# Kernel tuning notes

Measured on AMD Instinct MI355X. Metric: run time of the kernel, lower is better.

The kernel has to match this reference:

```python
import jax, jax.numpy as jnp
import numpy as np

DIM = 3
N = DIM * DIM          # 9 digits
NUM_NODES = N * N      # 81 cells
HID = 96
EMB = 16

def sudoku_edges():
    edges = []
    for r in range(N):
        for c in range(N):
            s = set()
            for k in range(N):
                s.add(r * N + k)
                s.add(k * N + c)
            br, bc = (r // DIM) * DIM, (c // DIM) * DIM
            for dr in range(DIM):
                for dc in range(DIM):
                    s.add((br + dr) * N + (bc + dc))
            s.discard(r * N + c)
            edges.append(sorted(s))
    return np.asarray(edges, np.int32)  # (81, 20)

EDGES = jnp.asarray(sudoku_edges())

def mlp(x, params):
    # ReLU between hidden layers, no activation after the last layer
    for w, b in params[:-1]:
        x = jax.nn.relu(x @ w + b)
    w, b = params[-1]
    return x @ w + b

def setup_inputs():
    key = jax.random.key(0)
    ks = iter(jax.random.split(key, 64))
    B = 256
    def p(shape, scale=0.1):
        return jax.random.normal(next(ks), shape, jnp.float32) * scale
    inp = {}
    inp['grids'] = jax.random.randint(next(ks), (B, NUM_NODES), 0, 3)
    inp['iters'] = 8
    inp['emb'] = p((3, EMB))
    inp['in_w0'] = p((EMB, HID)); inp['in_b0'] = jnp.zeros((HID,), jnp.float32)
    inp['in_w1'] = p((HID, HID)); inp['in_b1'] = jnp.zeros((HID,), jnp.float32)
    inp['in_w2'] = p((HID, HID)); inp['in_b2'] = jnp.zeros((HID,), jnp.float32)
    inp['rel_w0'] = p((2 * HID, HID)); inp['rel_b0'] = jnp.zeros((HID,), jnp.float32)
    inp['rel_w1'] = p((HID, HID)); inp['rel_b1'] = jnp.zeros((HID,), jnp.float32)
    inp['rel_w2'] = p((HID, HID)); inp['rel_b2'] = jnp.zeros((HID,), jnp.float32)
    inp['g_w0'] = p((2 * HID, HID)); inp['g_b0'] = jnp.zeros((HID,), jnp.float32)
    inp['g_w1'] = p((HID, HID)); inp['g_b1'] = jnp.zeros((HID,), jnp.float32)
    inp['g_w2'] = p((HID, HID)); inp['g_b2'] = jnp.zeros((HID,), jnp.float32)
    inp['lstm_wih'] = p((HID, 4 * HID)); inp['lstm_whh'] = p((HID, 4 * HID))
    inp['lstm_bih'] = jnp.zeros((4 * HID,), jnp.float32)
    inp['lstm_bhh'] = jnp.zeros((4 * HID,), jnp.float32)
    inp['r_w0'] = p((HID, HID)); inp['r_b0'] = jnp.zeros((HID,), jnp.float32)
    inp['r_w1'] = p((HID, HID)); inp['r_b1'] = jnp.zeros((HID,), jnp.float32)
    inp['r_w2'] = p((HID, N)); inp['r_b2'] = jnp.zeros((N,), jnp.float32)
    inp['c0'] = p((B * NUM_NODES, HID), 1.0)  # torch.randn LSTM cell init
    return inp

def reference(grids, iters, emb, in_w0, in_b0, in_w1, in_b1, in_w2, in_b2,
              rel_w0, rel_b0, rel_w1, rel_b1, rel_w2, rel_b2,
              g_w0, g_b0, g_w1, g_b1, g_w2, g_b2,
              lstm_wih, lstm_whh, lstm_bih, lstm_bhh,
              r_w0, r_b0, r_w1, r_b1, r_w2, r_b2, c0):
    B = grids.shape[0]
    in_p = [(in_w0, in_b0), (in_w1, in_b1), (in_w2, in_b2)]
    rel_p = [(rel_w0, rel_b0), (rel_w1, rel_b1), (rel_w2, rel_b2)]
    g_p = [(g_w0, g_b0), (g_w1, g_b1), (g_w2, g_b2)]
    r_p = [(r_w0, r_b0), (r_w1, r_b1), (r_w2, r_b2)]
    X = mlp(emb[grids], in_p)                     # (B, 81, 96)
    H0 = jax.lax.stop_gradient(X)                 # X.clone().detach()
    h = H0.reshape(B * NUM_NODES, HID)
    bias = lstm_bih + lstm_bhh

    def step(carry, _):
        h, c = carry
        Hn = h.reshape(B, NUM_NODES, HID)
        nbr = Hn[:, EDGES]                        # (B, 81, 20, 96) neighbor gather
        self_f = jnp.broadcast_to(Hn[:, :, None], nbr.shape)
        msgs = mlp(jnp.concatenate([self_f, nbr], axis=-1), rel_p)
        M = msgs.sum(axis=2)                      # scatter-sum of messages
        x_in = mlp(jnp.concatenate([X, M], axis=-1), g_p).reshape(B * NUM_NODES, HID)
        gates = x_in @ lstm_wih + h @ lstm_whh + bias
        i, f, g, o = jnp.split(gates, 4, axis=-1)  # torch gate order i,f,g,o
        c2 = jax.nn.sigmoid(f) * c + jax.nn.sigmoid(i) * jnp.tanh(g)
        h2 = jax.nn.sigmoid(o) * jnp.tanh(c2)
        out = mlp(h2.reshape(B, NUM_NODES, HID), r_p)  # (B, 81, 9)
        return (h2, c2), out

    _, outputs = jax.lax.scan(step, (h, c0), None, length=iters)
    return outputs  # (iters, B, 81, 9)
```

## Files before the change

kernel.cpp:

```cpp
#include <hip/hip_runtime.h>
#include <hip/hip_bf16.h>
#include <stdint.h>

typedef __attribute__((ext_vector_type(8))) short short8v;
typedef __attribute__((ext_vector_type(4))) float float4v;

#define DEVI __device__ __forceinline__

constexpr int BATCH = 256;
constexpr int NN   = 81;
constexpr int HID  = 96;
constexpr int NOUT = 9;
constexpr int BLOCK = 512;
constexpr int LDA = 100;
constexpr int LDB = 104;

constexpr int OFF_XG = 0;
constexpr int OFF_H0 = 7776;
constexpr int OFF_H1 = 11988;
constexpr int OFF_MS = 16200;
constexpr int OFF_AP = 24300;
constexpr int OFF_BV = 32400;
constexpr int SMEM_F = 40500;

constexpr int W_REL0A = 0;
constexpr int W_REL0B = 18432;
constexpr int W_REL1  = 36864;
constexpr int W_COMB  = 55296;
constexpr int W_G1    = 73728;
constexpr int W_IHC   = 92160;
constexpr int W_HH    = 165888;
constexpr int W_R0    = 239616;
constexpr int W_R1    = 258048;
constexpr int W_R2    = 276480;
constexpr int W_IN1   = 279552;
constexpr int W_IN2   = 297984;
constexpr int W_G0A   = 316416;
constexpr int BC2OFF  = 334848;
constexpr int B3OFF   = 335616;

DEVI float sigm(float x)  { return 1.f / (1.f + __expf(-x)); }
DEVI float tanh_(float x) { return 1.f - 2.f / (__expf(2.f * x) + 1.f); }

DEVI short bfhi(float x) { union { float f; unsigned u; } v; v.f = x; return (short)(v.u >> 16); }
DEVI float fromBits(short s) { union { unsigned u; float f; } v; v.u = ((unsigned)(unsigned short)s) << 16; return v.f; }
DEVI short bfrne(float x) {
  union { float f; unsigned u; } v; v.f = x;
  unsigned r = v.u + 0x7fffu + ((v.u >> 16) & 1u);
  return (short)(r >> 16);
}
DEVI void split1(float x, short& h, short& l) { h = bfhi(x); l = bfrne(x - fromBits(h)); }

DEVI void packFrag(const float* p, short8v& v) {
  const float4 a = *reinterpret_cast<const float4*>(p);
  const float4 b = *reinterpret_cast<const float4*>(p + 4);
  v[0] = bfrne(a.x); v[1] = bfrne(a.y); v[2] = bfrne(a.z); v[3] = bfrne(a.w);
  v[4] = bfrne(b.x); v[5] = bfrne(b.y); v[6] = bfrne(b.z); v[7] = bfrne(b.w);
}
DEVI void packFragPair(const float* ap, const float* bp, short8v& v) {
  const float4 a0 = *reinterpret_cast<const float4*>(ap);
  const float4 a1 = *reinterpret_cast<const float4*>(ap + 4);
  const float4 b0 = *reinterpret_cast<const float4*>(bp);
  const float4 b1 = *reinterpret_cast<const float4*>(bp + 4);
  v[0] = bfrne(fmaxf(a0.x + b0.x, 0.f)); v[1] = bfrne(fmaxf(a0.y + b0.y, 0.f));
  v[2] = bfrne(fmaxf(a0.z + b0.z, 0.f)); v[3] = bfrne(fmaxf(a0.w + b0.w, 0.f));
  v[4] = bfrne(fmaxf(a1.x + b1.x, 0.f)); v[5] = bfrne(fmaxf(a1.y + b1.y, 0.f));
  v[6] = bfrne(fmaxf(a1.z + b1.z, 0.f)); v[7] = bfrne(fmaxf(a1.w + b1.w, 0.f));
}

DEVI float4v mfma2(short8v a, short8v bh, short8v bl, float4v acc) {
  acc = __builtin_amdgcn_mfma_f32_16x16x32_bf16(a, bh, acc, 0, 0, 0);
  acc = __builtin_amdgcn_mfma_f32_16x16x32_bf16(a, bl, acc, 0, 0, 0);
  return acc;
}

DEVI int nbr_of(int n, int e) {
  const int r = n / 9, c = n - 9 * r;
  if (e < 8)  { int cc = c + 1 + e;  if (cc >= 9) cc -= 9; return r * 9 + cc; }
  if (e < 16) { int rr = r + e - 7;  if (rr >= 9) rr -= 9; return rr * 9 + c; }
  const int q = e - 16, dr = 1 + (q >> 1), dc = 1 + (q & 1);
  const int rm = r % 3, cm = c % 3;
  int rr = r - rm + rm + dr; rr -= (rm + dr >= 3) ? 3 : 0;
  int cc = c - cm + cm + dc; cc -= (cm + dc >= 3) ? 3 : 0;
  return rr * 9 + cc;
}

__global__ __launch_bounds__(64)
void pack_kernel(const float* rel_w0, const float* rel_w1, const float* rel_w2,
                 const float* g_w0, const float* g_w1, const float* g_w2,
                 const float* wih, const float* whh,
                 const float* r_w0, const float* r_w1, const float* r_w2,
                 const float* in_w1, const float* in_w2,
                 const float* rel_b2, const float* g_b2, short* ws)
{
  const int lane = threadIdx.x;
  const int blk = blockIdx.x;
  if (blk == 327) {
    float* bc2 = reinterpret_cast<float*>(ws + BC2OFF);
    float* b3  = reinterpret_cast<float*>(ws + B3OFF);
    for (int c = lane; c < 384; c += 64) {
      float a = 0.f;
      for (int t = 0; t < 96; ++t) a += g_b2[t] * wih[t * 384 + c];
      bc2[c] = a;
    }
    for (int c = lane; c < 96; c += 64) {
      float a = 0.f;
      for (int t = 0; t < 96; ++t) a += 20.f * rel_b2[t] * g_w0[(96 + t) * 96 + c];
      b3[c] = a;
    }
    return;
  }
  const int starts[14] = {0,18,36,54,72,90,162,234,252,270,273,291,309,327};
  int mi = 0;
  while (blk >= starts[mi + 1]) ++mi;
  const int tt = blk - starts[mi];
  const int ntile = starts[mi + 1] - starts[mi];
  const int kt = tt % 3, ct = tt / 3;
  const int q = lane >> 4, r = lane & 15;
  int off, C = 96, row0 = 0;
  const float* src = nullptr;
  switch (mi) {
    case 0:  src = rel_w0; off = W_REL0A; break;
    case 1:  src = rel_w0; row0 = 96; off = W_REL0B; break;
    case 2:  src = rel_w1; off = W_REL1; break;
    case 3:  off = W_COMB; break;
    case 4:  src = g_w1; off = W_G1; break;
    case 5:  C = 384; off = W_IHC; break;
    case 6:  src = whh; C = 384; off = W_HH; break;
    case 7:  src = r_w0; off = W_R0; break;
    case 8:  src = r_w1; off = W_R1; break;
    case 9:  src = r_w2; C = 9; off = W_R2; break;
    case 10: src = in_w1; off = W_IN1; break;
    case 11: src = in_w2; off = W_IN2; break;
    default: src = g_w0; off = W_G0A; break;
  }
  const int c = ct * 16 + r;
  short* hd = ws + off + tt * 512 + lane * 8;
  short* ld = hd + ntile * 512;
  if (mi == 3 || mi == 5) {
    const float* A  = (mi == 3) ? rel_w2 : g_w2;
    const float* Bm = (mi == 3) ? (g_w0 + 96 * 96) : wih;
    const int C2 = (mi == 3) ? 96 : 384;
    float acc[8] = {0,0,0,0,0,0,0,0};
    for (int t = 0; t < 96; ++t) {
      const float bv = Bm[t * C2 + c];
      #pragma unroll
      for (int j = 0; j < 8; ++j) acc[j] += A[(kt * 32 + q * 8 + j) * 96 + t] * bv;
    }
    #pragma unroll
    for (int j = 0; j < 8; ++j) { short h, l; split1(acc[j], h, l); hd[j] = h; ld[j] = l; }
  } else {
    #pragma unroll
    for (int j = 0; j < 8; ++j) {
      const int k = row0 + kt * 32 + q * 8 + j;
      float w = (c < C) ? src[k * C + c] : 0.f;
      short h, l; split1(w, h, l);
      hd[j] = h; ld[j] = l;
    }
  }
}

template<bool ABF, bool OBF, bool RELU, bool XGADD>
DEVI void stage96(float* sm, int aOff, const short* WS, int wOff, int wTiles,
                  const float* bias, float bscale, int dOff, int dstLDf,
                  int wave, int lane)
{
  const int rl = lane & 15, q = lane >> 4;
  const int plane = wTiles * 512;
  const short* asb = reinterpret_cast<const short*>(sm + aOff);
  short* dsb = reinterpret_cast<short*>(sm + dOff);
  float* dsf = sm + dOff;
  #pragma unroll 1
  for (int t = wave; t < 18; t += 8) {
    const int rtp = t % 3, ct = t / 3;
    short8v a2[2][3];
    #pragma unroll
    for (int sub = 0; sub < 2; ++sub) {
      const int row = rtp * 32 + sub * 16 + rl;
      if (ABF) {
        const short* ap = asb + row * LDB + q * 8;
        #pragma unroll
        for (int kt = 0; kt < 3; ++kt)
          a2[sub][kt] = *reinterpret_cast<const short8v*>(ap + kt * 32);
      } else {
        const float* ap = &sm[aOff + row * LDA + q * 8];
        #pragma unroll
        for (int kt = 0; kt < 3; ++kt) packFrag(ap + kt * 32, a2[sub][kt]);
      }
    }
    float4v acc0 = {0.f, 0.f, 0.f, 0.f}, acc1 = {0.f, 0.f, 0.f, 0.f};
    #pragma unroll
    for (int kt = 0; kt < 3; ++kt) {
      const short* bp = WS + wOff + (ct * 3 + kt) * 512 + lane * 8;
      const short8v bh = *reinterpret_cast<const short8v*>(bp);
      const short8v bl = *reinterpret_cast<const short8v*>(bp + plane);
      acc0 = mfma2(a2[0][kt], bh, bl, acc0);
      acc1 = mfma2(a2[1][kt], bh, bl, acc1);
    }
    const int col = ct * 16 + rl;
    #pragma unroll
    for (int sub = 0; sub < 2; ++sub) {
      #pragma unroll
      for (int j = 0; j < 4; ++j) {
        const int row = rtp * 32 + sub * 16 + q * 4 + j;
        if (row < NN) {
          float v = sub ? acc1[j] : acc0[j];
          if (bias)  v += bias[col] * bscale;
          if (XGADD) v += sm[OFF_XG + row * 96 + col];
          if (RELU)  v = fmaxf(v, 0.f);
          if (OBF) dsb[row * LDB + col] = bfrne(v);
          else     dsf[row * dstLDf + col] = v;
        }
      }
    }
  }
}

__global__ __launch_bounds__(BLOCK) __attribute__((amdgpu_waves_per_eu(1, 2)))
void rrn_kernel(const int* __restrict__ grids, const int* __restrict__ itersp,
                const float* __restrict__ emb, const float* __restrict__ in_w0,
                const float* __restrict__ in_b0, const float* __restrict__ in_b1,
                const float* __restrict__ in_b2,
                const float* __restrict__ rel_b0, const float* __restrict__ rel_b1,
                const float* __restrict__ g_b0, const float* __restrict__ g_b1,
                const float* __restrict__ bih, const float* __restrict__ bhh,
                const float* __restrict__ r_b0, const float* __restrict__ r_b1,
                const float* __restrict__ r_b2,
                const float* __restrict__ c0, const short* __restrict__ WS,
                float* __restrict__ out)
{
  __shared__ float sm[SMEM_F];
  const int b = blockIdx.x, tid = threadIdx.x;
  const int wave = tid >> 6, lane = tid & 63;
  const int rl = lane & 15, q = lane >> 4;
  const int iters = itersp[0];

  float creg[6][4];
  #pragma unroll
  for (int rt = 0; rt < 6; ++rt)
    #pragma unroll
    for (int j = 0; j < 4; ++j) creg[rt][j] = 0.f;
  if (wave < 6) {
    #pragma unroll
    for (int rt = 0; rt < 6; ++rt) {
      #pragma unroll
      for (int j = 0; j < 4; ++j) {
        const int n = rt * 16 + q * 4 + j, col = wave * 16 + rl;
        creg[rt][j] = (n < NN) ? c0[(size_t)b * NN * HID + n * HID + col] : 0.f;
      }
    }
  }

  for (int t = tid; t < NN * HID; t += BLOCK) {
    const int n = t / HID, col = t - n * HID;
    const int g = grids[b * NN + n];
    float acc = in_b0[col];
    #pragma unroll
    for (int k = 0; k < 16; ++k) acc += emb[g * 16 + k] * in_w0[k * HID + col];
    sm[OFF_AP + n * LDA + col] = fmaxf(acc, 0.f);
  }
  __syncthreads();
  stage96<false, true, true,  false>(sm, OFF_AP, WS, W_IN1, 18, in_b1, 1.f, OFF_MS, 0, wave, lane);
  __syncthreads();
  stage96<true,  true, false, false>(sm, OFF_MS, WS, W_IN2, 18, in_b2, 1.f, OFF_H0, 0, wave, lane);
  __syncthreads();
  stage96<true, false, false, false>(sm, OFF_H0, WS, W_G0A, 18, g_b0,  1.f, OFF_XG, 96, wave, lane);
  __syncthreads();

  const float* b3ptr = reinterpret_cast<const float*>(WS + B3OFF);
  const float* bc2   = reinterpret_cast<const float*>(WS + BC2OFF);

  for (int it = 0; it < iters; ++it) {
    const int hc = (it & 1) ? OFF_H1 : OFF_H0;
    const int hn = (it & 1) ? OFF_H0 : OFF_H1;

    for (int i = tid; i < 8100; i += BLOCK) sm[OFF_MS + i] = 0.f;
    stage96<true, false, false, false>(sm, hc, WS, W_REL0A, 18, rel_b0, 1.f, OFF_AP, LDA, wave, lane);
    stage96<true, false, false, false>(sm, hc, WS, W_REL0B, 18, nullptr, 0.f, OFF_BV, LDA, wave, lane);
    __syncthreads();

    #pragma unroll 1
    for (int g2 = wave; g2 < 51; g2 += 8) {
      short8v a2[2][3];
      #pragma unroll
      for (int sub = 0; sub < 2; ++sub) {
        const int row = g2 * 32 + sub * 16 + rl;
        if (row < 1620) {
          const int n = row / 20, e = row - 20 * n, m = nbr_of(n, e);
          const float* ap = &sm[OFF_AP + n * LDA + q * 8];
          const float* bp = &sm[OFF_BV + m * LDA + q * 8];
          #pragma unroll
          for (int kt = 0; kt < 3; ++kt)
            packFragPair(ap + kt * 32, bp + kt * 32, a2[sub][kt]);
        } else {
          const short8v z = {0,0,0,0,0,0,0,0};
          #pragma unroll
          for (int kt = 0; kt < 3; ++kt) a2[sub][kt] = z;
        }
      }
      #pragma unroll 1
      for (int ct = 0; ct < 6; ++ct) {
        const float rb1c = rel_b1[ct * 16 + rl];
        float4v acc0 = {0,0,0,0}, acc1 = {0,0,0,0};
        #pragma unroll
        for (int kt = 0; kt < 3; ++kt) {
          const short* bp = WS + W_REL1 + (ct * 3 + kt) * 512 + lane * 8;
          const short8v bh = *reinterpret_cast<const short8v*>(bp);
          const short8v bl = *reinterpret_cast<const short8v*>(bp + 18 * 512);
          acc0 = mfma2(a2[0][kt], bh, bl, acc0);
          acc1 = mfma2(a2[1][kt], bh, bl, acc1);
        }
        const int col = ct * 16 + rl;
        #pragma unroll
        for (int sub = 0; sub < 2; ++sub) {
          const int r0 = g2 * 32 + sub * 16 + q * 4;
          if (r0 < 1620) {
            const int node = r0 / 20;
            const float4v a = sub ? acc1 : acc0;
            const float s = fmaxf(a[0] + rb1c, 0.f) + fmaxf(a[1] + rb1c, 0.f)
                          + fmaxf(a[2] + rb1c, 0.f) + fmaxf(a[3] + rb1c, 0.f);
            atomicAdd(&sm[OFF_MS + node * LDA + col], s);
          }
        }
        __builtin_amdgcn_sched_barrier(0);
      }
    }
    __syncthreads();

    stage96<false, true, true, true>(sm, OFF_MS, WS, W_COMB, 18, b3ptr, 1.f, OFF_AP, 0, wave, lane);
    __syncthreads();
    stage96<true, true, true, false>(sm, OFF_AP, WS, W_G1, 18, g_b1, 1.f, OFF_MS, 0, wave, lane);
    __syncthreads();

    if (wave < 6) {
      const int colh = wave * 16 + rl;
      const float bI = bih[colh]       + bhh[colh]       + bc2[colh];
      const float bF = bih[96 + colh]  + bhh[96 + colh]  + bc2[96 + colh];
      const float bG = bih[192 + colh] + bhh[192 + colh] + bc2[192 + colh];
      const float bO = bih[288 + colh] + bhh[288 + colh] + bc2[288 + colh];
      const short* xs = reinterpret_cast<const short*>(sm + OFF_MS);
      const short* hs = reinterpret_cast<const short*>(sm + hc);
      short* hnp = reinterpret_cast<short*>(sm + hn);
      #pragma unroll
      for (int rt = 0; rt < 6; ++rt) {
        const int row = rt * 16 + rl;
        short8v af[6];
        #pragma unroll
        for (int kt = 0; kt < 3; ++kt)
          af[kt] = *reinterpret_cast<const short8v*>(xs + row * LDB + kt * 32 + q * 8);
        #pragma unroll
        for (int kt = 3; kt < 6; ++kt)
          af[kt] = *reinterpret_cast<const short8v*>(hs + row * LDB + (kt - 3) * 32 + q * 8);
        float4v ga[4];
        #pragma unroll
        for (int gate = 0; gate < 4; ++gate) {
          const int ct = gate * 6 + wave;
          float4v acc = {0.f, 0.f, 0.f, 0.f};
          #pragma unroll
          for (int kt = 0; kt < 3; ++kt) {
            const short* bp = WS + W_IHC + (ct * 3 + kt) * 512 + lane * 8;
            acc = mfma2(af[kt], *reinterpret_cast<const short8v*>(bp),
                        *reinterpret_cast<const short8v*>(bp + 72 * 512), acc);
          }
          __builtin_amdgcn_sched_barrier(0);
          #pragma unroll
          for (int kt = 3; kt < 6; ++kt) {
            const short* bp = WS + W_HH + (ct * 3 + kt - 3) * 512 + lane * 8;
            acc = mfma2(af[kt], *reinterpret_cast<const short8v*>(bp),
                        *reinterpret_cast<const short8v*>(bp + 72 * 512), acc);
          }
          ga[gate] = acc;
          __builtin_amdgcn_sched_barrier(0);
        }
        #pragma unroll
        for (int j = 0; j < 4; ++j) {
          const int n = rt * 16 + q * 4 + j;
          const float gi = ga[0][j] + bI;
          const float gf = ga[1][j] + bF;
          const float gg = ga[2][j] + bG;
          const float go = ga[3][j] + bO;
          const float c2 = sigm(gf) * creg[rt][j] + sigm(gi) * tanh_(gg);
          creg[rt][j] = c2;
          if (n < NN) hnp[n * LDB + colh] = bfrne(sigm(go) * tanh_(c2));
        }
      }
    }
    __syncthreads();

    stage96<true, true, true, false>(sm, hn, WS, W_R0, 18, r_b0, 1.f, OFF_AP, 0, wave, lane);
    __syncthreads();
    stage96<true, true, true, false>(sm, OFF_AP, WS, W_R1, 18, r_b1, 1.f, OFF_MS, 0, wave, lane);
    __syncthreads();
    if (wave < 6) {
      const int rt6 = wave;
      const short* asb = reinterpret_cast<const short*>(sm + OFF_MS);
      const int row = rt6 * 16 + rl;
      short8v a2[3];
      #pragma unroll
      for (int kt = 0; kt < 3; ++kt)
        a2[kt] = *reinterpret_cast<const short8v*>(asb + row * LDB + kt * 32 + q * 8);
      float4v acc = {0,0,0,0};
      #pragma unroll
      for (int kt = 0; kt < 3; ++kt) {
        const short* bp = WS + W_R2 + kt * 512 + lane * 8;
        acc = mfma2(a2[kt], *reinterpret_cast<const short8v*>(bp),
                    *reinterpret_cast<const short8v*>(bp + 3 * 512), acc);
      }
      if (rl < NOUT) {
        float* op = out + ((size_t)it * BATCH + b) * NN * NOUT;
        #pragma unroll
        for (int j = 0; j < 4; ++j) {
          const int r2 = rt6 * 16 + q * 4 + j;
          if (r2 < NN) op[r2 * NOUT + rl] = acc[j] + r_b2[rl];
        }
      }
    }
    __syncthreads();
  }
}

extern "C" void kernel_launch(void* const* d_in, const int* in_sizes, int n_in,
                              void* d_out, int out_size, void* d_ws, size_t ws_size,
                              hipStream_t stream) {
  (void)in_sizes; (void)n_in; (void)out_size; (void)ws_size;
  const int* grids = (const int*)d_in[0];
  const int* iters = (const int*)d_in[1];
  const float *emb = (const float*)d_in[2],
    *in_w0 = (const float*)d_in[3],  *in_b0 = (const float*)d_in[4],
    *in_w1 = (const float*)d_in[5],  *in_b1 = (const float*)d_in[6],
    *in_w2 = (const float*)d_in[7],  *in_b2 = (const float*)d_in[8],
    *rel_w0 = (const float*)d_in[9],  *rel_b0 = (const float*)d_in[10],
    *rel_w1 = (const float*)d_in[11], *rel_b1 = (const float*)d_in[12],
    *rel_w2 = (const float*)d_in[13], *rel_b2 = (const float*)d_in[14],
    *g_w0 = (const float*)d_in[15], *g_b0 = (const float*)d_in[16],
    *g_w1 = (const float*)d_in[17], *g_b1 = (const float*)d_in[18],
    *g_w2 = (const float*)d_in[19], *g_b2 = (const float*)d_in[20],
    *wih = (const float*)d_in[21], *whh = (const float*)d_in[22],
    *bih = (const float*)d_in[23], *bhh = (const float*)d_in[24],
    *r_w0 = (const float*)d_in[25], *r_b0 = (const float*)d_in[26],
    *r_w1 = (const float*)d_in[27], *r_b1 = (const float*)d_in[28],
    *r_w2 = (const float*)d_in[29], *r_b2 = (const float*)d_in[30],
    *c0 = (const float*)d_in[31];
  short* ws = (short*)d_ws;
  pack_kernel<<<dim3(328), dim3(64), 0, stream>>>(
      rel_w0, rel_w1, rel_w2, g_w0, g_w1, g_w2, wih, whh,
      r_w0, r_w1, r_w2, in_w1, in_w2, rel_b2, g_b2, ws);
  rrn_kernel<<<dim3(BATCH), dim3(BLOCK), 0, stream>>>(
      grids, iters, emb, in_w0, in_b0, in_b1, in_b2,
      rel_b0, rel_b1, g_b0, g_b1,
      bih, bhh, r_b0, r_b1, r_b2, c0, (const short*)ws, (float*)d_out);
}
```

Baseline: 785.5 us.

## Defer readout MLP to a separate batched kernel using hidden-state history

The recurrent kernel now writes each iteration's bf16 hidden state to a workspace history buffer and skips the three-layer readout MLP inside its serial loop. A new readout kernel launched over (batch, iters) blocks recomputes the readout from that history in parallel. This takes two stage GEMMs and their syncs off the critical path of the 256-block recurrent loop, which uses only 256 workgroups. In exchange it adds global traffic for the history plus a second launch, and it falls back to the old path if the workspace is too small.

```diff
diff --git a/kernel.cpp b/kernel.cpp
--- a/kernel.cpp
+++ b/kernel.cpp
@@ -38,6 +38,7 @@
 constexpr int W_G0A   = 316416;
 constexpr int BC2OFF  = 334848;
 constexpr int B3OFF   = 335616;
+constexpr int HISTOFF = 335808;
 
 DEVI float sigm(float x)  { return 1.f / (1.f + __expf(-x)); }
 DEVI float tanh_(float x) { return 1.f - 2.f / (__expf(2.f * x) + 1.f); }
@@ -216,6 +217,7 @@
   }
 }
 
+template<bool DEFER>
 __global__ __launch_bounds__(BLOCK) __attribute__((amdgpu_waves_per_eu(1, 2)))
 void rrn_kernel(const int* __restrict__ grids, const int* __restrict__ itersp,
                 const float* __restrict__ emb, const float* __restrict__ in_w0,
@@ -227,7 +229,7 @@
                 const float* __restrict__ r_b0, const float* __restrict__ r_b1,
                 const float* __restrict__ r_b2,
                 const float* __restrict__ c0, const short* __restrict__ WS,
-                float* __restrict__ out)
+                short* __restrict__ hist, float* __restrict__ out)
 {
   __shared__ float sm[SMEM_F];
   const int b = blockIdx.x, tid = threadIdx.x;
@@ -341,6 +343,7 @@
       const short* xs = reinterpret_cast<const short*>(sm + OFF_MS);
       const short* hs = reinterpret_cast<const short*>(sm + hc);
       short* hnp = reinterpret_cast<short*>(sm + hn);
+      short* hg = hist + (size_t)(it * BATCH + b) * (NN * HID);
       #pragma unroll
       for (int rt = 0; rt < 6; ++rt) {
         const int row = rt * 16 + rl;
@@ -381,48 +384,106 @@
           const float go = ga[3][j] + bO;
           const float c2 = sigm(gf) * creg[rt][j] + sigm(gi) * tanh_(gg);
           creg[rt][j] = c2;
-          if (n < NN) hnp[n * LDB + colh] = bfrne(sigm(go) * tanh_(c2));
+          if (n < NN) {
+            const short hb = bfrne(sigm(go) * tanh_(c2));
+            hnp[n * LDB + colh] = hb;
+            if (DEFER) hg[n * HID + colh] = hb;
+          }
         }
       }
     }
     __syncthreads();
 
-    stage96<true, true, true, false>(sm, hn, WS, W_R0, 18, r_b0, 1.f, OFF_AP, 0, wave, lane);
-    __syncthreads();
-    stage96<true, true, true, false>(sm, OFF_AP, WS, W_R1, 18, r_b1, 1.f, OFF_MS, 0, wave, lane);
-    __syncthreads();
-    if (wave < 6) {
-      const int rt6 = wave;
-      const short* asb = reinterpret_cast<const short*>(sm + OFF_MS);
-      const int row = rt6 * 16 + rl;
-      short8v a2[3];
+    if constexpr (!DEFER) {
+      stage96<true, true, true, false>(sm, hn, WS, W_R0, 18, r_b0, 1.f, OFF_AP, 0, wave, lane);
+      __syncthreads();
+      stage96<true, true, true, false>(sm, OFF_AP, WS, W_R1, 18, r_b1, 1.f, OFF_MS, 0, wave, lane);
+      __syncthreads();
+      if (wave < 6) {
+        const int rt6 = wave;
+        const short* asb = reinterpret_cast<const short*>(sm + OFF_MS);
+        const int row = rt6 * 16 + rl;
+        short8v a2[3];
+        #pragma unroll
+        for (int kt = 0; kt < 3; ++kt)
+          a2[kt] = *reinterpret_cast<const short8v*>(asb + row * LDB + kt * 32 + q * 8);
+        float4v acc = {0,0,0,0};
+        #pragma unroll
+        for (int kt = 0; kt < 3; ++kt) {
+          const short* bp = WS + W_R2 + kt * 512 + lane * 8;
+          acc = mfma2(a2[kt], *reinterpret_cast<const short8v*>(bp),
+                      *reinterpret_cast<const short8v*>(bp + 3 * 512), acc);
+        }
+        if (rl < NOUT) {
+          float* op = out + ((size_t)it * BATCH + b) * NN * NOUT;
+          #pragma unroll
+          for (int j = 0; j < 4; ++j) {
+            const int r2 = rt6 * 16 + q * 4 + j;
+            if (r2 < NN) op[r2 * NOUT + rl] = acc[j] + r_b2[rl];
+          }
+        }
+      }
+      __syncthreads();
+    }
+  }
+}
+
+constexpr int RO_H  = 0;
+constexpr int RO_B1 = 4212;
+constexpr int RO_B2 = 8424;
+constexpr int RO_F  = 13416;
+
+__global__ __launch_bounds__(BLOCK)
+void readout_kernel(const short* __restrict__ hist, const short* __restrict__ WS,
+                    const float* __restrict__ r_b0, const float* __restrict__ r_b1,
+                    const float* __restrict__ r_b2, float* __restrict__ out)
+{
+  __shared__ float sm[RO_F];
+  const int b = blockIdx.x, it = blockIdx.y;
+  const int tid = threadIdx.x, wave = tid >> 6, lane = tid & 63;
+  const int rl = lane & 15, q = lane >> 4;
+
+  short* hx = reinterpret_cast<short*>(sm + RO_H);
+  const short* src = hist + (size_t)(it * BATCH + b) * (NN * HID);
+  for (int t = tid; t < NN * HID; t += BLOCK) {
+    const int n = t / HID, c = t - n * HID;
+    hx[n * LDB + c] = src[t];
+  }
+  __syncthreads();
+  stage96<true, true, true, false>(sm, RO_H,  WS, W_R0, 18, r_b0, 1.f, RO_B1, 0, wave, lane);
+  __syncthreads();
+  stage96<true, true, true, false>(sm, RO_B1, WS, W_R1, 18, r_b1, 1.f, RO_B2, 0, wave, lane);
+  __syncthreads();
+  if (wave < 6) {
+    const int rt6 = wave;
+    const short* asb = reinterpret_cast<const short*>(sm + RO_B2);
+    const int row = rt6 * 16 + rl;
+    short8v a2[3];
+    #pragma unroll
+    for (int kt = 0; kt < 3; ++kt)
+      a2[kt] = *reinterpret_cast<const short8v*>(asb + row * LDB + kt * 32 + q * 8);
+    float4v acc = {0,0,0,0};
+    #pragma unroll
+    for (int kt = 0; kt < 3; ++kt) {
+      const short* bp = WS + W_R2 + kt * 512 + lane * 8;
+      acc = mfma2(a2[kt], *reinterpret_cast<const short8v*>(bp),
+                  *reinterpret_cast<const short8v*>(bp + 3 * 512), acc);
+    }
+    if (rl < NOUT) {
+      float* op = out + ((size_t)it * BATCH + b) * NN * NOUT;
       #pragma unroll
-      for (int kt = 0; kt < 3; ++kt)
-        a2[kt] = *reinterpret_cast<const short8v*>(asb + row * LDB + kt * 32 + q * 8);
-      float4v acc = {0,0,0,0};
-      #pragma unroll
-      for (int kt = 0; kt < 3; ++kt) {
-        const short* bp = WS + W_R2 + kt * 512 + lane * 8;
-        acc = mfma2(a2[kt], *reinterpret_cast<const short8v*>(bp),
-                    *reinterpret_cast<const short8v*>(bp + 3 * 512), acc);
-      }
-      if (rl < NOUT) {
-        float* op = out + ((size_t)it * BATCH + b) * NN * NOUT;
-        #pragma unroll
-        for (int j = 0; j < 4; ++j) {
-          const int r2 = rt6 * 16 + q * 4 + j;
-          if (r2 < NN) op[r2 * NOUT + rl] = acc[j] + r_b2[rl];
-        }
-      }
-    }
-    __syncthreads();
+      for (int j = 0; j < 4; ++j) {
+        const int r2 = rt6 * 16 + q * 4 + j;
+        if (r2 < NN) op[r2 * NOUT + rl] = acc[j] + r_b2[rl];
+      }
+    }
   }
 }
 
 extern "C" void kernel_launch(void* const* d_in, const int* in_sizes, int n_in,
                               void* d_out, int out_size, void* d_ws, size_t ws_size,
                               hipStream_t stream) {
-  (void)in_sizes; (void)n_in; (void)out_size; (void)ws_size;
+  (void)in_sizes; (void)n_in;
   const int* grids = (const int*)d_in[0];
   const int* iters = (const int*)d_in[1];
   const float *emb = (const float*)d_in[2],
@@ -442,11 +503,25 @@
     *r_w2 = (const float*)d_in[29], *r_b2 = (const float*)d_in[30],
     *c0 = (const float*)d_in[31];
   short* ws = (short*)d_ws;
+  short* hist = ws + HISTOFF;
+  const int iters_h = out_size / (BATCH * NN * NOUT);
+  const size_t need = ((size_t)HISTOFF + (size_t)iters_h * BATCH * NN * HID) * sizeof(short);
+  const bool defer = ws_size >= need && iters_h > 0;
+
   pack_kernel<<<dim3(328), dim3(64), 0, stream>>>(
       rel_w0, rel_w1, rel_w2, g_w0, g_w1, g_w2, wih, whh,
       r_w0, r_w1, r_w2, in_w1, in_w2, rel_b2, g_b2, ws);
-  rrn_kernel<<<dim3(BATCH), dim3(BLOCK), 0, stream>>>(
-      grids, iters, emb, in_w0, in_b0, in_b1, in_b2,
-      rel_b0, rel_b1, g_b0, g_b1,
-      bih, bhh, r_b0, r_b1, r_b2, c0, (const short*)ws, (float*)d_out);
-}
+  if (defer) {
+    rrn_kernel<true><<<dim3(BATCH), dim3(BLOCK), 0, stream>>>(
+        grids, iters, emb, in_w0, in_b0, in_b1, in_b2,
+        rel_b0, rel_b1, g_b0, g_b1,
+        bih, bhh, r_b0, r_b1, r_b2, c0, (const short*)ws, hist, (float*)d_out);
+    readout_kernel<<<dim3(BATCH, iters_h), dim3(BLOCK), 0, stream>>>(
+        hist, (const short*)ws, r_b0, r_b1, r_b2, (float*)d_out);
+  } else {
+    rrn_kernel<false><<<dim3(BATCH), dim3(BLOCK), 0, stream>>>(
+        grids, iters, emb, in_w0, in_b0, in_b1, in_b2,
+        rel_b0, rel_b1, g_b0, g_b1,
+        bih, bhh, r_b0, r_b1, r_b2, c0, (const short*)ws, hist, (float*)d_out);
+  }
+}
```

Measured after the change: 784.3 us. Within noise of the previous version (-0.2%).
